# Kernel optimization log

Hardware: AMD Instinct MI355X
Metric: run time of the kernel (lower is better)

Reference implementation:

```python
import jax, jax.numpy as jnp
import numpy as np


def setup_inputs() -> dict:
    key = jax.random.key(0)
    ks = jax.random.split(key, 6)
    B, N, D, E = 16, 64, 256, 256
    nodes = jax.random.normal(ks[0], (B * N, D), jnp.float32)
    edges = jax.random.normal(ks[1], (B * N * N, E), jnp.float32)
    W_in = jax.random.normal(ks[2], (2 * D + E, D), jnp.float32) / np.float32(np.sqrt(2 * D + E))
    b_in = jnp.zeros((D,), jnp.float32)
    W_coef = jax.random.normal(ks[3], (D, 1), jnp.float32) / np.float32(np.sqrt(D))
    b_coef = jnp.zeros((1,), jnp.float32)
    W_out = jax.random.normal(ks[4], (D, D), jnp.float32) / np.float32(np.sqrt(D))
    b_out = jnp.zeros((D,), jnp.float32)
    return {"nodes": nodes, "edges": edges, "W_in": W_in, "b_in": b_in,
            "W_coef": W_coef, "b_coef": b_coef, "W_out": W_out, "b_out": b_out,
            "B": B, "N": N}


def reference(nodes, edges, W_in, b_in, W_coef, b_coef, W_out, b_out, B, N):
    # Uniform nums = [N]*B special case of the ragged torch loop.
    D = nodes.shape[-1]
    n3 = nodes.reshape(B, N, D)
    # pair[b,i,j] = [node_i, node_j, edge_ij]  -> [B,N,N,2D+E]
    pair = jnp.concatenate([
        jnp.broadcast_to(n3[:, :, None, :], (B, N, N, D)),
        jnp.broadcast_to(n3[:, None, :, :], (B, N, N, D)),
        edges.reshape(B, N, N, -1),
    ], axis=-1)
    h = jax.nn.relu(pair @ W_in + b_in)            # [B,N,N,D]
    coefs = h @ W_coef + b_coef                    # [B,N,N,1]
    diag = jnp.eye(N, dtype=coefs.dtype)[None, :, :, None] * jnp.float32(1e9)
    attn = jax.nn.softmax(coefs - diag, axis=2)    # softmax over j, diag masked
    residual = jnp.sum(attn * h, axis=2)           # [B,N,D]
    new_nodes = nodes + jax.nn.relu(residual.reshape(B * N, D) @ W_out + b_out)
    return new_nodes, h.reshape(B * N * N, D)
```

## Files before the change

### kernel.cpp

```cpp
#include <hip/hip_runtime.h>
#include <hip/hip_bf16.h>

typedef unsigned int u32;
typedef unsigned short u16;
typedef __attribute__((ext_vector_type(8))) short bf16x8;
typedef __attribute__((ext_vector_type(4))) float f32x4;
typedef __attribute__((ext_vector_type(4))) float f4;

#define DI __device__ __forceinline__

DI u16 f2bfu(float f){
  union{float f; u32 i;} u; u.f = f;
  u32 lsb = (u.i >> 16) & 1u;
  u.i += 0x7fffu + lsb;
  return (u16)(u.i >> 16);
}

union BU { uint4 v; bf16x8 s; };

DI void gld16(const void* g, void* l){
  __builtin_amdgcn_global_load_lds(
      (const __attribute__((address_space(1))) void*)g,
      (__attribute__((address_space(3))) void*)l, 16, 0, 0);
}

__global__ __launch_bounds__(256) void k_pack(const float* __restrict__ W_in,
                                              u16* __restrict__ Wp3,
                                              u16* __restrict__ Wp12)
{
  int idx = blockIdx.x * 256 + threadIdx.x;
  int l = idx & 63;
  int g = idx >> 6;
  int lq = l >> 4, lr = l & 15;
  u16 o[8];
  if (g < 128){
    int nt = g >> 3, kk = g & 7;
    int n  = nt * 16 + lr;
    int k0 = 512 + kk * 32 + lq * 8;
#pragma unroll
    for (int tt = 0; tt < 8; tt++) o[tt] = f2bfu(W_in[(size_t)(k0 + tt) * 256 + n]);
    *(uint4*)(Wp3 + (size_t)idx * 8) = *(uint4*)o;
  } else {
    int g2 = g - 128;
    int half = g2 >> 7, rem = g2 & 127;
    int nt = rem >> 3, kk = rem & 7;
    int n  = nt * 16 + lr;
    int k0 = half * 256 + kk * 32 + lq * 8;
#pragma unroll
    for (int tt = 0; tt < 8; tt++) o[tt] = f2bfu(W_in[(size_t)(k0 + tt) * 256 + n]);
    *(uint4*)(Wp12 + (size_t)g2 * 512 + (size_t)l * 8) = *(uint4*)o;
  }
}

__global__ __launch_bounds__(256) void k_pre(
    const float* __restrict__ nodes, const float* __restrict__ b_in,
    const u16* __restrict__ Wp12, float* __restrict__ P1, float* __restrict__ P2)
{
  const int t = threadIdx.x;
  const int w = t >> 6, l = t & 63, lq = l >> 4, lr = l & 15;
  const int bid = blockIdx.x;
  const int rt = bid >> 3, half = (bid >> 2) & 1, cg = bid & 3;

  bf16x8 af[8];
  {
    const float* ap = nodes + (size_t)(rt * 64 + 16 * w + lr) * 256 + lq * 8;
#pragma unroll
    for (int kk = 0; kk < 8; kk++){
      float4 x = *(const float4*)(ap + kk * 32);
      float4 y = *(const float4*)(ap + kk * 32 + 4);
      bf16x8 a;
      a[0]=(short)f2bfu(x.x); a[1]=(short)f2bfu(x.y); a[2]=(short)f2bfu(x.z); a[3]=(short)f2bfu(x.w);
      a[4]=(short)f2bfu(y.x); a[5]=(short)f2bfu(y.y); a[6]=(short)f2bfu(y.z); a[7]=(short)f2bfu(y.w);
      af[kk] = a;
    }
  }
  const uint4* wp = (const uint4*)(Wp12 + (size_t)half * 128 * 512);
  float* P = half ? P2 : P1;
#pragma unroll
  for (int ntl = 0; ntl < 4; ntl++){
    const int nt = cg * 4 + ntl;
    f32x4 acc = {0.f, 0.f, 0.f, 0.f};
#pragma unroll
    for (int kk = 0; kk < 8; kk++){
      BU bu; bu.v = wp[(nt * 8 + kk) * 64 + l];
      acc = __builtin_amdgcn_mfma_f32_16x16x32_bf16(af[kk], bu.s, acc, 0, 0, 0);
    }
    const int col = nt * 16 + lr;
    const float bv = half ? 0.f : b_in[col];
#pragma unroll
    for (int r = 0; r < 4; r++){
      const int row = rt * 64 + 16 * w + 4 * lq + r;
      P[(size_t)row * 256 + col] = acc[r] + bv;
    }
  }
}

__global__ __launch_bounds__(256, 3) void k_h(
    const float* __restrict__ edges, const u16* __restrict__ Wp3,
    const float* __restrict__ W_coef, const float* __restrict__ P1,
    const float* __restrict__ P2, float* __restrict__ out_h,
    float* __restrict__ coefW)
{
  __shared__ uint4 wS[2][1024];

  const int t = threadIdx.x;
  const int w = t >> 6, l = t & 63, lq = l >> 4, lr = l & 15;
  const int bid = blockIdx.x;
  const int bi = ((bid & 7) << 7) | (bid >> 3);
  const int b = bi >> 6;
  const int j = 16 * w + lr;

  const char* wp3b = (const char*)Wp3;
  auto stage = [&](int bufi, int ntc){
    const char* src = wp3b + (size_t)ntc * 16384;
    char* dst = (char*)&wS[bufi][0];
#pragma unroll
    for (int c = 0; c < 4; ++c)
      gld16(src + (w * 4 + c) * 1024 + l * 16, dst + (w * 4 + c) * 1024);
  };

  stage(0, 0);

  bf16x8 af[8];
  {
    const float* ap = edges + (size_t)bi * 16384 + (size_t)j * 256 + lq * 8;
    float4 x[4], y[4];
#pragma unroll
    for (int kk = 0; kk < 4; kk++){
      x[kk] = *(const float4*)(ap + kk * 32);
      y[kk] = *(const float4*)(ap + kk * 32 + 4);
    }
#pragma unroll
    for (int kk = 0; kk < 4; kk++){
      bf16x8 a;
      a[0]=(short)f2bfu(x[kk].x); a[1]=(short)f2bfu(x[kk].y); a[2]=(short)f2bfu(x[kk].z); a[3]=(short)f2bfu(x[kk].w);
      a[4]=(short)f2bfu(y[kk].x); a[5]=(short)f2bfu(y[kk].y); a[6]=(short)f2bfu(y[kk].z); a[7]=(short)f2bfu(y[kk].w);
      af[kk] = a;
    }
#pragma unroll
    for (int kk = 0; kk < 4; kk++){
      x[kk] = *(const float4*)(ap + (kk + 4) * 32);
      y[kk] = *(const float4*)(ap + (kk + 4) * 32 + 4);
    }
#pragma unroll
    for (int kk = 0; kk < 4; kk++){
      bf16x8 a;
      a[0]=(short)f2bfu(x[kk].x); a[1]=(short)f2bfu(x[kk].y); a[2]=(short)f2bfu(x[kk].z); a[3]=(short)f2bfu(x[kk].w);
      a[4]=(short)f2bfu(y[kk].x); a[5]=(short)f2bfu(y[kk].y); a[6]=(short)f2bfu(y[kk].z); a[7]=(short)f2bfu(y[kk].w);
      af[kk + 4] = a;
    }
  }

  const float* p1p = P1 + (size_t)bi * 256;
  const float* p2p = P2 + ((size_t)b * 64 + j) * 256;
  float* hop = out_h + ((size_t)bi * 64 + j) * 256;
  float cpart = 0.f;

  __syncthreads();
  int buf = 0;
#pragma unroll
  for (int ntc = 0; ntc < 8; ntc++){
    if (ntc < 7) stage(buf ^ 1, ntc + 1);
#pragma unroll
    for (int nt2 = 0; nt2 < 2; nt2++){
      const int nt = ntc * 2 + nt2;
      f32x4 acc = {0.f, 0.f, 0.f, 0.f};
#pragma unroll
      for (int kk = 0; kk < 8; kk++){
        BU bu; bu.v = wS[buf][(nt2 * 8 + kk) * 64 + l];
        acc = __builtin_amdgcn_mfma_f32_16x16x32_bf16(bu.s, af[kk], acc, 0, 0, 0);
      }
      const int d0 = nt * 16 + 4 * lq;
      f4 p1v = *(const f4*)(p1p + d0);
      f4 p2v = *(const f4*)(p2p + d0);
      f4 wcv = *(const f4*)(W_coef + d0);
      f4 h;
#pragma unroll
      for (int r = 0; r < 4; r++){
        float xx = acc[r] + p1v[r] + p2v[r];
        h[r] = xx > 0.f ? xx : 0.f;
      }
      *(f4*)(hop + d0) = h;
      cpart += h[0]*wcv[0] + h[1]*wcv[1] + h[2]*wcv[2] + h[3]*wcv[3];
    }
    __syncthreads();
    buf ^= 1;
  }

  cpart += __shfl_xor(cpart, 16, 64);
  cpart += __shfl_xor(cpart, 32, 64);
  if (lq == 0) coefW[(size_t)bi * 64 + j] = cpart;
}

__global__ __launch_bounds__(256) void k_soft(
    const float* __restrict__ coefW, const float* __restrict__ b_coef,
    float* __restrict__ attnW)
{
  const int t = threadIdx.x;
  const int w = t >> 6, l = t & 63;
  const int bi = blockIdx.x * 4 + w;
  const int i = bi & 63;
  float val = coefW[(size_t)bi * 64 + l] + b_coef[0] - (l == i ? 1e9f : 0.f);
  float m = val;
#pragma unroll
  for (int off = 32; off >= 1; off >>= 1){ float o = __shfl_xor(m, off, 64); m = m > o ? m : o; }
  float e = __expf(val - m);
  float s = e;
#pragma unroll
  for (int off = 32; off >= 1; off >>= 1) s += __shfl_xor(s, off, 64);
  attnW[(size_t)bi * 64 + l] = e / s;
}

__global__ __launch_bounds__(256, 4) void k_res(
    const float* __restrict__ attnW, const float* __restrict__ h_in,
    float* __restrict__ RES)
{
  __shared__ float attnS[64];
  __shared__ f4 resP[3][64];

  const int t = threadIdx.x;
  const int q = t >> 6, l = t & 63;
  const int bid = blockIdx.x;
  const int bi = ((bid & 7) << 7) | (bid >> 3);

  if (t < 64) attnS[t] = attnW[(size_t)bi * 64 + t];
  __syncthreads();

  const f4* hb = (const f4*)(h_in + (size_t)bi * 16384) + l;
  f4 sum = {0.f, 0.f, 0.f, 0.f};
#pragma unroll
  for (int jj = 0; jj < 16; jj++){
    const int j = jj * 4 + q;
    f4 v = hb[(size_t)j * 64];
    sum += attnS[j] * v;
  }
  if (q) resP[q - 1][l] = sum;
  __syncthreads();
  if (q == 0){
    f4 r = ((sum + resP[0][l]) + resP[1][l]) + resP[2][l];
    *((f4*)RES + (size_t)bi * 64 + l) = r;
  }
}

__global__ __launch_bounds__(256) void k_out(
    const float* __restrict__ nodes, const float* __restrict__ RES,
    const float* __restrict__ W_out, const float* __restrict__ b_out,
    float* __restrict__ out_nodes)
{
  __shared__ float sR[4][256];
  const int t = threadIdx.x;
  const int r0 = blockIdx.x * 4;
#pragma unroll
  for (int r = 0; r < 4; r++) sR[r][t] = RES[(size_t)(r0 + r) * 256 + t];
  __syncthreads();

  const float bv = b_out[t];
  float a0 = bv, a1 = bv, a2 = bv, a3 = bv;
#pragma unroll 8
  for (int k = 0; k < 256; k++){
    const float wv = W_out[(size_t)k * 256 + t];
    a0 += sR[0][k] * wv;
    a1 += sR[1][k] * wv;
    a2 += sR[2][k] * wv;
    a3 += sR[3][k] * wv;
  }
  out_nodes[(size_t)(r0 + 0) * 256 + t] = nodes[(size_t)(r0 + 0) * 256 + t] + (a0 > 0.f ? a0 : 0.f);
  out_nodes[(size_t)(r0 + 1) * 256 + t] = nodes[(size_t)(r0 + 1) * 256 + t] + (a1 > 0.f ? a1 : 0.f);
  out_nodes[(size_t)(r0 + 2) * 256 + t] = nodes[(size_t)(r0 + 2) * 256 + t] + (a2 > 0.f ? a2 : 0.f);
  out_nodes[(size_t)(r0 + 3) * 256 + t] = nodes[(size_t)(r0 + 3) * 256 + t] + (a3 > 0.f ? a3 : 0.f);
}

extern "C" void kernel_launch(void* const* d_in, const int* in_sizes, int n_in,
                              void* d_out, int out_size, void* d_ws, size_t ws_size,
                              hipStream_t stream)
{
  const float* nodes  = (const float*)d_in[0];
  const float* edges  = (const float*)d_in[1];
  const float* W_in   = (const float*)d_in[2];
  const float* b_in   = (const float*)d_in[3];
  const float* W_coef = (const float*)d_in[4];
  const float* b_coef = (const float*)d_in[5];
  const float* W_out  = (const float*)d_in[6];
  const float* b_out  = (const float*)d_in[7];
  (void)in_sizes; (void)n_in; (void)out_size; (void)ws_size;

  float* P1  = (float*)d_ws;
  float* P2  = P1 + 262144;
  u16*  Wp3  = (u16*)(P2 + 262144);
  u16*  Wp12 = Wp3 + 65536;
  float* coefW = (float*)(Wp12 + 131072);
  float* attnW = coefW + 65536;
  float* RES   = attnW + 65536;

  float* out_nodes = (float*)d_out;
  float* out_h = out_nodes + 262144;

  hipLaunchKernelGGL(k_pack, dim3(96),   dim3(256), 0, stream, W_in, Wp3, Wp12);
  hipLaunchKernelGGL(k_pre,  dim3(128),  dim3(256), 0, stream, nodes, b_in, Wp12, P1, P2);
  hipLaunchKernelGGL(k_h,    dim3(1024), dim3(256), 0, stream,
                     edges, Wp3, W_coef, P1, P2, out_h, coefW);
  hipLaunchKernelGGL(k_soft, dim3(256),  dim3(256), 0, stream, coefW, b_coef, attnW);
  hipLaunchKernelGGL(k_res,  dim3(1024), dim3(256), 0, stream, attnW, out_h, RES);
  hipLaunchKernelGGL(k_out,  dim3(256),  dim3(256), 0, stream,
                     nodes, RES, W_out, b_out, out_nodes);
}
```

Before: 185.1 us.

## Fuse softmax and attention-weighted residual into the h GEMM kernel

```diff
diff --git a/kernel.cpp b/kernel.cpp
--- a/kernel.cpp
+++ b/kernel.cpp
@@ -22,6 +22,14 @@
   __builtin_amdgcn_global_load_lds(
       (const __attribute__((address_space(1))) void*)g,
       (__attribute__((address_space(3))) void*)l, 16, 0, 0);
+}
+
+DI float redlr(float v){
+  v += __shfl_xor(v, 1, 64);
+  v += __shfl_xor(v, 2, 64);
+  v += __shfl_xor(v, 4, 64);
+  v += __shfl_xor(v, 8, 64);
+  return v;
 }
 
 __global__ __launch_bounds__(256) void k_pack(const float* __restrict__ W_in,
@@ -95,19 +103,22 @@
   }
 }
 
-__global__ __launch_bounds__(256, 3) void k_h(
+__global__ __launch_bounds__(256, 3) void k_main(
     const float* __restrict__ edges, const u16* __restrict__ Wp3,
-    const float* __restrict__ W_coef, const float* __restrict__ P1,
-    const float* __restrict__ P2, float* __restrict__ out_h,
-    float* __restrict__ coefW)
+    const float* __restrict__ W_coef, const float* __restrict__ b_coef,
+    const float* __restrict__ P1, const float* __restrict__ P2,
+    float* __restrict__ out_h, float* __restrict__ RES)
 {
   __shared__ uint4 wS[2][1024];
+  __shared__ float coefS[64];
+  __shared__ float attnS[64];
+  __shared__ float resW[4][256];
 
   const int t = threadIdx.x;
   const int w = t >> 6, l = t & 63, lq = l >> 4, lr = l & 15;
   const int bid = blockIdx.x;
   const int bi = ((bid & 7) << 7) | (bid >> 3);
-  const int b = bi >> 6;
+  const int b = bi >> 6, i = bi & 63;
   const int j = 16 * w + lr;
 
   const char* wp3b = (const char*)Wp3;
@@ -156,6 +167,10 @@
   float* hop = out_h + ((size_t)bi * 64 + j) * 256;
   float cpart = 0.f;
 
+  f32x4 acc[16];
+#pragma unroll
+  for (int nt = 0; nt < 16; nt++) acc[nt] = (f32x4){0.f, 0.f, 0.f, 0.f};
+
   __syncthreads();
   int buf = 0;
 #pragma unroll
@@ -164,11 +179,10 @@
 #pragma unroll
     for (int nt2 = 0; nt2 < 2; nt2++){
       const int nt = ntc * 2 + nt2;
-      f32x4 acc = {0.f, 0.f, 0.f, 0.f};
 #pragma unroll
       for (int kk = 0; kk < 8; kk++){
         BU bu; bu.v = wS[buf][(nt2 * 8 + kk) * 64 + l];
-        acc = __builtin_amdgcn_mfma_f32_16x16x32_bf16(bu.s, af[kk], acc, 0, 0, 0);
+        acc[nt] = __builtin_amdgcn_mfma_f32_16x16x32_bf16(bu.s, af[kk], acc[nt], 0, 0, 0);
       }
       const int d0 = nt * 16 + 4 * lq;
       f4 p1v = *(const f4*)(p1p + d0);
@@ -177,8 +191,10 @@
       f4 h;
 #pragma unroll
       for (int r = 0; r < 4; r++){
-        float xx = acc[r] + p1v[r] + p2v[r];
-        h[r] = xx > 0.f ? xx : 0.f;
+        float xx = acc[nt][r] + p1v[r] + p2v[r];
+        xx = xx > 0.f ? xx : 0.f;
+        h[r] = xx;
+        acc[nt][r] = xx;
       }
       *(f4*)(hop + d0) = h;
       cpart += h[0]*wcv[0] + h[1]*wcv[1] + h[2]*wcv[2] + h[3]*wcv[3];
@@ -189,57 +205,35 @@
 
   cpart += __shfl_xor(cpart, 16, 64);
   cpart += __shfl_xor(cpart, 32, 64);
-  if (lq == 0) coefW[(size_t)bi * 64 + j] = cpart;
-}
-
-__global__ __launch_bounds__(256) void k_soft(
-    const float* __restrict__ coefW, const float* __restrict__ b_coef,
-    float* __restrict__ attnW)
-{
-  const int t = threadIdx.x;
-  const int w = t >> 6, l = t & 63;
-  const int bi = blockIdx.x * 4 + w;
-  const int i = bi & 63;
-  float val = coefW[(size_t)bi * 64 + l] + b_coef[0] - (l == i ? 1e9f : 0.f);
-  float m = val;
-#pragma unroll
-  for (int off = 32; off >= 1; off >>= 1){ float o = __shfl_xor(m, off, 64); m = m > o ? m : o; }
-  float e = __expf(val - m);
-  float s = e;
-#pragma unroll
-  for (int off = 32; off >= 1; off >>= 1) s += __shfl_xor(s, off, 64);
-  attnW[(size_t)bi * 64 + l] = e / s;
-}
-
-__global__ __launch_bounds__(256, 4) void k_res(
-    const float* __restrict__ attnW, const float* __restrict__ h_in,
-    float* __restrict__ RES)
-{
-  __shared__ float attnS[64];
-  __shared__ f4 resP[3][64];
-
-  const int t = threadIdx.x;
-  const int q = t >> 6, l = t & 63;
-  const int bid = blockIdx.x;
-  const int bi = ((bid & 7) << 7) | (bid >> 3);
-
-  if (t < 64) attnS[t] = attnW[(size_t)bi * 64 + t];
-  __syncthreads();
-
-  const f4* hb = (const f4*)(h_in + (size_t)bi * 16384) + l;
-  f4 sum = {0.f, 0.f, 0.f, 0.f};
-#pragma unroll
-  for (int jj = 0; jj < 16; jj++){
-    const int j = jj * 4 + q;
-    f4 v = hb[(size_t)j * 64];
-    sum += attnS[j] * v;
-  }
-  if (q) resP[q - 1][l] = sum;
-  __syncthreads();
-  if (q == 0){
-    f4 r = ((sum + resP[0][l]) + resP[1][l]) + resP[2][l];
-    *((f4*)RES + (size_t)bi * 64 + l) = r;
-  }
+  if (lq == 0) coefS[j] = cpart;
+  __syncthreads();
+
+  if (t < 64){
+    int jj = t;
+    float val = coefS[jj] + b_coef[0] - (jj == i ? 1e9f : 0.f);
+    float m = val;
+#pragma unroll
+    for (int off = 32; off >= 1; off >>= 1){ float o = __shfl_xor(m, off, 64); m = m > o ? m : o; }
+    float e = __expf(val - m);
+    float s = e;
+#pragma unroll
+    for (int off = 32; off >= 1; off >>= 1) s += __shfl_xor(s, off, 64);
+    attnS[jj] = e / s;
+  }
+  __syncthreads();
+
+  {
+    const float a = attnS[j];
+#pragma unroll
+    for (int nt = 0; nt < 16; nt++){
+      f4 part;
+#pragma unroll
+      for (int r = 0; r < 4; r++) part[r] = redlr(a * acc[nt][r]);
+      if (lr == 0) *(f4*)&resW[w][nt * 16 + 4 * lq] = part;
+    }
+  }
+  __syncthreads();
+  RES[(size_t)bi * 256 + t] = resW[0][t] + resW[1][t] + resW[2][t] + resW[3][t];
 }
 
 __global__ __launch_bounds__(256) void k_out(
@@ -288,19 +282,15 @@
   float* P2  = P1 + 262144;
   u16*  Wp3  = (u16*)(P2 + 262144);
   u16*  Wp12 = Wp3 + 65536;
-  float* coefW = (float*)(Wp12 + 131072);
-  float* attnW = coefW + 65536;
-  float* RES   = attnW + 65536;
+  float* RES = (float*)(Wp12 + 131072);
 
   float* out_nodes = (float*)d_out;
   float* out_h = out_nodes + 262144;
 
   hipLaunchKernelGGL(k_pack, dim3(96),   dim3(256), 0, stream, W_in, Wp3, Wp12);
   hipLaunchKernelGGL(k_pre,  dim3(128),  dim3(256), 0, stream, nodes, b_in, Wp12, P1, P2);
-  hipLaunchKernelGGL(k_h,    dim3(1024), dim3(256), 0, stream,
-                     edges, Wp3, W_coef, P1, P2, out_h, coefW);
-  hipLaunchKernelGGL(k_soft, dim3(256),  dim3(256), 0, stream, coefW, b_coef, attnW);
-  hipLaunchKernelGGL(k_res,  dim3(1024), dim3(256), 0, stream, attnW, out_h, RES);
+  hipLaunchKernelGGL(k_main, dim3(1024), dim3(256), 0, stream,
+                     edges, Wp3, W_coef, b_coef, P1, P2, out_h, RES);
   hipLaunchKernelGGL(k_out,  dim3(256),  dim3(256), 0, stream,
                      nodes, RES, W_out, b_out, out_nodes);
 }
```

After: 184.4 us. No clear change (-0.4%).
